# Kernel tuning notes

Hardware: AMD Instinct MI355X
Metric: run time of the kernel (lower is better)

Reference implementation:

```python
import jax, jax.numpy as jnp
import numpy as np

B, S, E = 4, 2048, 1024
H = 4
DH = E // H          # 256 head dim
DQ = E // 4          # 256 quaternion d_model
ALPHA = 1.5
EPS = 1e-10
FOCUS = 0.9
SEL = 2.0


def setup_inputs() -> dict:
    key = jax.random.key(0)
    ks = jax.random.split(key, 6)
    sc = 0.02
    return {
        "x": jax.random.normal(ks[0], (B, S, E), dtype=jnp.float32),
        "in_proj_w": jax.random.normal(ks[1], (3 * E, E), dtype=jnp.float32) * sc,
        "in_proj_b": jnp.zeros((3 * E,), dtype=jnp.float32),
        "out_w": jax.random.normal(ks[2], (E, E), dtype=jnp.float32) * sc,
        "out_b": jnp.zeros((E,), dtype=jnp.float32),
        "m_w1": jax.random.normal(ks[3], (E, E), dtype=jnp.float32) * sc,
        "m_b1": jnp.zeros((E,), dtype=jnp.float32),
        "m_w2": jax.random.normal(ks[4], (E, E), dtype=jnp.float32) * sc,
        "m_b2": jnp.zeros((E,), dtype=jnp.float32),
    }


def quaternion_multiply(q1, q2):
    # Hamilton product over last dim of size 4 (complex-valued components).
    w1, x1, y1, z1 = q1[..., 0], q1[..., 1], q1[..., 2], q1[..., 3]
    w2, x2, y2, z2 = q2[..., 0], q2[..., 1], q2[..., 2], q2[..., 3]
    return jnp.stack([
        w1 * w2 - x1 * x2 - y1 * y2 - z1 * z2,
        w1 * x2 + x1 * w2 + y1 * z2 - z1 * y2,
        w1 * y2 - x1 * z2 + y1 * w2 + z1 * x2,
        w1 * z2 + x1 * y2 - y1 * x2 + z1 * w2,
    ], axis=-1)


def _mha(x, in_proj_w, in_proj_b, out_w, out_b):
    # torch nn.MultiheadAttention self-attention, batch_first
    qkv = x @ in_proj_w.T + in_proj_b              # [B,S,3E]
    q, k, v = jnp.split(qkv, 3, axis=-1)
    q = q.reshape(B, S, H, DH)
    k = k.reshape(B, S, H, DH)
    v = v.reshape(B, S, H, DH)
    scores = jnp.einsum('bqhd,bkhd->bhqk', q, k) / jnp.sqrt(jnp.float32(DH))
    attn = jax.nn.softmax(scores, axis=-1)
    out = jnp.einsum('bhqk,bkhd->bqhd', attn, v).reshape(B, S, E)
    return out @ out_w.T + out_b


def _spectral_attention(signal):
    sq = signal.reshape(B, S, DQ, 4)
    sfft = jnp.fft.fft(sq, axis=-3)                 # complex64, FFT over seq
    kk = jnp.arange(S, dtype=jnp.float32)
    filt = jnp.exp(1j * ALPHA * jnp.arctan(jnp.log(kk + EPS)))  # [S] complex
    sf = sfft * filt[None, :, None, None]
    inter = quaternion_multiply(quaternion_multiply(sf, sf), sf)
    attended = jnp.fft.ifft(inter, axis=-3).real
    return attended.reshape(B, S, E)


def reference(x, in_proj_w, in_proj_b, out_w, out_b, m_w1, m_b1, m_w2, m_b2):
    nicotinic = _mha(x, in_proj_w, in_proj_b, out_w, out_b)
    h = jax.nn.gelu(x @ m_w1.T + m_b1, approximate=False)
    muscarinic = h @ m_w2.T + m_b2
    chol = FOCUS * nicotinic + (1.0 - FOCUS) * muscarinic
    attn_w = _spectral_attention(chol * SEL)
    return x * attn_w
```

## Files before the change

kernel.cpp:

```cpp
#include <hip/hip_runtime.h>
#include <cstdint>

typedef _Float16 f16;
typedef unsigned short u16;
typedef __attribute__((ext_vector_type(8))) _Float16 half8;
typedef __attribute__((ext_vector_type(4))) _Float16 half4;
typedef __attribute__((ext_vector_type(2))) __fp16 fp16x2;
typedef __attribute__((ext_vector_type(4))) float f32x4;

#define MFMA_F16(a, b, c) __builtin_amdgcn_mfma_f32_16x16x32_f16(a, b, c, 0, 0, 0)

#define WAITVM8() asm volatile("s_waitcnt vmcnt(8)" ::: "memory")
#define WAITVM4() asm volatile("s_waitcnt vmcnt(4)" ::: "memory")
#define WAITVM0() asm volatile("s_waitcnt vmcnt(0)" ::: "memory")
#define BARRIER() do { asm volatile("" ::: "memory"); __builtin_amdgcn_s_barrier(); \
                       asm volatile("" ::: "memory"); } while (0)

#define SCQ 0.09016844005555896f

__device__ inline void stage16(const void* g, void* l) {
#if defined(__has_builtin) && __has_builtin(__builtin_amdgcn_global_load_lds)
  __builtin_amdgcn_global_load_lds(
      (const __attribute__((address_space(1))) unsigned*)g,
      (__attribute__((address_space(3))) unsigned*)l, 16, 0, 0);
#else
  *(int4*)l = *(const int4*)g;
#endif
}

__device__ inline int pack_f16(float a, float b) {
#if defined(__has_builtin) && __has_builtin(__builtin_amdgcn_cvt_pkrtz)
  union { fp16x2 h; int i; } u;
  u.h = __builtin_amdgcn_cvt_pkrtz(a, b);
  return u.i;
#else
  union { f16 h[2]; int i; } u;
  u.h[0] = (f16)a; u.h[1] = (f16)b;
  return u.i;
#endif
}

__global__ __launch_bounds__(256)
void conv_all(const float* __restrict__ x, const float* __restrict__ wqkv,
              const float* __restrict__ w1, const float* __restrict__ wout,
              const float* __restrict__ w2, f16* __restrict__ dst,
              float2* __restrict__ tab) {
  if (blockIdx.x >= 7168) {
    int kk = (blockIdx.x - 7168) * 256 + threadIdx.x;
    if (kk < 2048) {
      float s, c;
      sincosf(1.5f * atanf(logf((float)kk + 1e-10f)), &s, &c);
      tab[kk] = make_float2(c, s);
    } else if (kk < 3072) {
      int j = kk - 2048;
      float s, c;
      sincosf(-6.2831853071795864769f * (float)j * (1.0f / 2048.0f), &s, &c);
      tab[kk] = make_float2(c, s);
    }
    return;
  }
  int i = (blockIdx.x * 256 + threadIdx.x) * 8;
  const float* src; size_t dofs; float sc = 1.0f;
  if (i < 8388608)       { src = x + i;               dofs = i; }
  else if (i < 11534336) {
    int t = i - 8388608;
    src = wqkv + t; dofs = i;
    if ((t >> 10) < 1024) sc = SCQ;
  }
  else if (i < 12582912) { src = w1 + (i - 11534336);  dofs = i; }
  else if (i < 13631488) {
    int t = i - 12582912; int j = t >> 10, k = t & 1023;
    src = wout + t; dofs = 12582912 + (size_t)j * 2048 + k; sc = 1.8f;
  } else {
    int t = i - 13631488; int j = t >> 10, k = t & 1023;
    src = w2 + t; dofs = 13631488 - 1048576 + (size_t)j * 2048 + 1024 + k; sc = 0.2f;
  }
  float4 a = *(const float4*)src;
  float4 b = *(const float4*)(src + 4);
  half8 h;
  h[0] = (f16)(a.x * sc); h[1] = (f16)(a.y * sc); h[2] = (f16)(a.z * sc); h[3] = (f16)(a.w * sc);
  h[4] = (f16)(b.x * sc); h[5] = (f16)(b.y * sc); h[6] = (f16)(b.z * sc); h[7] = (f16)(b.w * sc);
  *(half8*)(dst + dofs) = h;
}

template<int EPI>
__global__ __launch_bounds__(256, 2)
void gemm_f16(const f16* __restrict__ A, const f16* __restrict__ W,
              const float* __restrict__ bias0, const float* __restrict__ bias1,
              void* __restrict__ out0, void* __restrict__ out1,
              f16* __restrict__ Vt, int N, int K) {
  __shared__ __align__(16) f16 lds[2][16384];
  const int tid = threadIdx.x;
  const int lane = tid & 63, w = tid >> 6;
  const int g = lane >> 4, lm = lane & 15;
  const int wr = w >> 1, wc = w & 1;
  const int nwg = gridDim.x * gridDim.y;
  const int flat = blockIdx.y * gridDim.x + blockIdx.x;
  const int logical = (flat & 7) * (nwg >> 3) + (flat >> 3);
  const int bx = logical % gridDim.x, by = logical / gridDim.x;
  const int m0 = by * 128, n0 = bx * 128;

  const f16* src[8];
#pragma unroll
  for (int j = 0; j < 8; ++j) {
    int u = j * 256 + tid;
    if (u < 1024) {
      int row = u >> 3, s = u & 7;
      src[j] = A + (size_t)(m0 + row) * K + ((s ^ (row & 7)) << 3);
    } else {
      int v = u - 1024;
      int row = v >> 3, s = v & 7;
      src[j] = W + (size_t)(n0 + row) * K + ((s ^ (row & 7)) << 3);
    }
  }

  f32x4 acc[4][4];
#pragma unroll
  for (int mt = 0; mt < 4; ++mt)
#pragma unroll
    for (int nt = 0; nt < 4; ++nt) acc[mt][nt] = (f32x4){0.f, 0.f, 0.f, 0.f};

#pragma unroll
  for (int j = 0; j < 8; ++j) stage16(src[j], &lds[0][(j * 256 + tid) * 8]);
  __syncthreads();

  const int KT = K >> 6;
#pragma unroll 1
  for (int t = 0; t < KT; ++t) {
    const f16* bufA = lds[t & 1];
    const f16* bufB = bufA + 8192;
    if (t + 1 < KT) {
#pragma unroll
      for (int j = 0; j < 8; ++j) {
        src[j] += 64;
        stage16(src[j], &lds[(t + 1) & 1][(j * 256 + tid) * 8]);
      }
      WAITVM8();
    } else {
      WAITVM0();
    }
    BARRIER();
#pragma unroll
    for (int ks = 0; ks < 2; ++ks) {
      half8 a[4], b[4];
#pragma unroll
      for (int mt = 0; mt < 4; ++mt) {
        int row = wr * 64 + mt * 16 + lm;
        a[mt] = *(const half8*)(bufA + row * 64 + (((ks * 4 + g) ^ (row & 7)) << 3));
      }
#pragma unroll
      for (int nt = 0; nt < 4; ++nt) {
        int row = wc * 64 + nt * 16 + lm;
        b[nt] = *(const half8*)(bufB + row * 64 + (((ks * 4 + g) ^ (row & 7)) << 3));
      }
#pragma unroll
      for (int mt = 0; mt < 4; ++mt)
#pragma unroll
        for (int nt = 0; nt < 4; ++nt)
          acc[mt][nt] = MFMA_F16(a[mt], b[nt], acc[mt][nt]);
    }
    BARRIER();
  }

  const int crow = m0 + wr * 64 + g * 4;
  const int ccol = n0 + wc * 64 + lm;
  if (EPI == 3) {
    if (n0 < 2048) {
      f16* qk = (f16*)out0;
      const float bsc = (n0 < 1024) ? SCQ : 1.0f;
#pragma unroll
      for (int nt = 0; nt < 4; ++nt) {
        float bb = bias0[ccol + nt * 16] * bsc;
#pragma unroll
        for (int mt = 0; mt < 4; ++mt)
#pragma unroll
          for (int r = 0; r < 4; ++r)
            qk[(size_t)(crow + mt * 16 + r) * 3072 + ccol + nt * 16] =
                (f16)(acc[mt][nt][r] + bb);
      }
    } else if (n0 < 3072) {
      f16* ldsT = (f16*)lds;
#pragma unroll
      for (int nt = 0; nt < 4; ++nt) {
        float bb = bias0[ccol + nt * 16];
        int c = wc * 64 + nt * 16 + lm;
#pragma unroll
        for (int mt = 0; mt < 4; ++mt) {
          int r = wr * 64 + mt * 16 + g * 4;
#pragma unroll
          for (int rr = 0; rr < 4; ++rr)
            ldsT[c * 136 + r + rr] = (f16)(acc[mt][nt][rr] + bb);
        }
      }
      BARRIER();
      const int vbase0 = n0 - 2048;
      const int b = m0 >> 11, srow = m0 & 2047;
#pragma unroll
      for (int it = 0; it < 8; ++it) {
        int id = it * 256 + tid;
        int c = id >> 4, rb = id & 15;
        int vcol = vbase0 + c;
        int h = vcol >> 8, d = vcol & 255;
        half8 v = *(half8*)&ldsT[c * 136 + rb * 8];
        *(half8*)&Vt[(((size_t)(b * 4 + h)) * 256 + d) * 2048 + srow + rb * 8] = v;
      }
    } else {
      f16* cat = (f16*)out1;
      const int hc = ccol - 3072;
#pragma unroll
      for (int nt = 0; nt < 4; ++nt) {
        float bb = bias1[hc + nt * 16];
#pragma unroll
        for (int mt = 0; mt < 4; ++mt)
#pragma unroll
          for (int r = 0; r < 4; ++r) {
            float v = acc[mt][nt][r] + bb;
            v = 0.5f * v * (1.0f + erff(v * 0.70710678118654752f));
            cat[(size_t)(crow + mt * 16 + r) * 2048 + 1024 + hc + nt * 16] = (f16)v;
          }
      }
    }
  } else {
    f16* ldsT = (f16*)lds;
#pragma unroll
    for (int nt = 0; nt < 4; ++nt) {
      float bb = 1.8f * bias0[ccol + nt * 16] + 0.2f * bias1[ccol + nt * 16];
      int c = wc * 64 + nt * 16 + lm;
#pragma unroll
      for (int mt = 0; mt < 4; ++mt) {
        int r = wr * 64 + mt * 16 + g * 4;
#pragma unroll
        for (int rr = 0; rr < 4; ++rr)
          ldsT[c * 136 + r + rr] = (f16)(acc[mt][nt][rr] + bb);
      }
    }
    BARRIER();
    f16* ch = (f16*)out0;
#pragma unroll
    for (int it = 0; it < 8; ++it) {
      int id = it * 256 + tid;
      int c = id >> 4, rb = id & 15;
      half8 v = *(half8*)&ldsT[c * 136 + rb * 8];
      *(half8*)&ch[(size_t)(n0 + c) * 8192 + m0 + rb * 8] = v;
    }
  }
}

__global__ __launch_bounds__(512, 1)
void flash_f16(const f16* __restrict__ qkv, const f16* __restrict__ Vt,
               f16* __restrict__ attn) {
  __shared__ __align__(16) f16 lds[65536];
  const int tid = threadIdx.x;
  const int lane = tid & 63, w = tid >> 6;
  const int g = lane >> 4, lm = lane & 15;
  const int raw = blockIdx.x;
  const int bh = (raw & 7) * 2 + (raw >> 7);
  const int qt = (raw >> 3) & 15;
  const int b = bh >> 2, h = bh & 3;
  const int q0 = qt * 128 + w * 16;

  half8 qf[8];
  {
    const f16* qp = qkv + (size_t)(b * 2048 + q0 + lm) * 3072 + h * 256 + g * 8;
#pragma unroll
    for (int c = 0; c < 8; ++c) qf[c] = *(const half8*)(qp + c * 32);
  }

  const f16* kbase = qkv + (size_t)b * 2048 * 3072 + 1024 + h * 256;
  const f16* vbase = Vt + (size_t)bh * 256 * 2048;
  int kofs[4], vofs[4];
#pragma unroll
  for (int j = 0; j < 4; ++j) {
    int u = j * 512 + tid;
    int kv = u >> 5, s = u & 31;
    kofs[j] = kv * 3072 + ((s ^ (kv & 7)) << 3);
    int d = u >> 3, sl = u & 7;
    vofs[j] = d * 2048 + ((sl ^ (d & 7)) << 3);
  }

  f32x4 o[16];
#pragma unroll
  for (int f = 0; f < 16; ++f) o[f] = (f32x4){0.f, 0.f, 0.f, 0.f};
  float m = -3e38f, l = 0.f;
  half8 paP0 = (half8){0, 0, 0, 0, 0, 0, 0, 0};
  half8 paP1 = (half8){0, 0, 0, 0, 0, 0, 0, 0};

#pragma unroll
  for (int j = 0; j < 4; ++j) stage16(kbase + kofs[j], &lds[(j * 512 + tid) * 8]);

#pragma unroll 1
  for (int t = 0; t < 32; ++t) {
    const int cb_ = t & 1;
    if (t < 31) {
      const int kt = (t + 1) * 196608;
#pragma unroll
      for (int j = 0; j < 4; ++j)
        stage16(kbase + kofs[j] + kt, &lds[(cb_ ^ 1) * 16384 + (j * 512 + tid) * 8]);
    }
    {
      const int vt_ = t * 64;
#pragma unroll
      for (int j = 0; j < 4; ++j)
        stage16(vbase + vofs[j] + vt_, &lds[32768 + cb_ * 16384 + (j * 512 + tid) * 8]);
    }
    if (t < 31) { WAITVM8(); } else { WAITVM4(); }
    BARRIER();

    const f16* kb = &lds[cb_ * 16384];

    f32x4 s0 = {0.f, 0.f, 0.f, 0.f}, s1 = {0.f, 0.f, 0.f, 0.f};
    f32x4 s2 = {0.f, 0.f, 0.f, 0.f}, s3 = {0.f, 0.f, 0.f, 0.f};
    __builtin_amdgcn_s_setprio(1);
#pragma unroll
    for (int c = 0; c < 8; ++c) {
      int slot = ((c * 4 + g) ^ (lm & 7)) << 3;
      const f16* kr = kb + lm * 256 + slot;
      half8 b0 = *(const half8*)(kr);
      half8 b1 = *(const half8*)(kr + 16 * 256);
      half8 b2 = *(const half8*)(kr + 32 * 256);
      half8 b3 = *(const half8*)(kr + 48 * 256);
      s0 = MFMA_F16(b0, qf[c], s0);
      s1 = MFMA_F16(b1, qf[c], s1);
      s2 = MFMA_F16(b2, qf[c], s2);
      s3 = MFMA_F16(b3, qf[c], s3);
    }
    __builtin_amdgcn_s_setprio(0);

    if (t > 0) {
      const f16* vbp = &lds[32768 + (cb_ ^ 1) * 16384];
      __builtin_amdgcn_s_setprio(1);
#pragma unroll
      for (int f = 0; f < 16; ++f) {
        int d = f * 16 + lm;
        const f16* vr = vbp + d * 64;
        half8 bv0 = *(const half8*)(vr + ((g ^ (d & 7)) << 3));
        half8 bv1 = *(const half8*)(vr + (((4 + g) ^ (d & 7)) << 3));
        o[f] = MFMA_F16(paP0, bv0, o[f]);
        o[f] = MFMA_F16(paP1, bv1, o[f]);
      }
      __builtin_amdgcn_s_setprio(0);
    }

    float mx = fmaxf(fmaxf(fmaxf(s0[0], s0[1]), fmaxf(s0[2], s0[3])),
                     fmaxf(fmaxf(s1[0], s1[1]), fmaxf(s1[2], s1[3])));
    mx = fmaxf(mx, fmaxf(fmaxf(fmaxf(s2[0], s2[1]), fmaxf(s2[2], s2[3])),
                         fmaxf(fmaxf(s3[0], s3[1]), fmaxf(s3[2], s3[3]))));
    mx = fmaxf(mx, __shfl_xor(mx, 16));
    mx = fmaxf(mx, __shfl_xor(mx, 32));

    if (!__all(mx <= m + 8.0f)) {
      float mn = fmaxf(m, mx);
      float corr = exp2f(m - mn);
      m = mn; l *= corr;
#pragma unroll
      for (int r = 0; r < 4; ++r) {
        float cr = __shfl(corr, ((lane >> 2) & 12) + r);
#pragma unroll
        for (int f = 0; f < 16; ++f) o[f][r] *= cr;
      }
    }

    float e0[4], e1[4], e2[4], e3[4];
#pragma unroll
    for (int r = 0; r < 4; ++r) {
      e0[r] = exp2f(s0[r] - m);
      e1[r] = exp2f(s1[r] - m);
      e2[r] = exp2f(s2[r] - m);
      e3[r] = exp2f(s3[r] - m);
    }
    float rs = ((e0[0] + e0[1]) + (e0[2] + e0[3])) + ((e1[0] + e1[1]) + (e1[2] + e1[3]))
             + ((e2[0] + e2[1]) + (e2[2] + e2[3])) + ((e3[0] + e3[1]) + (e3[2] + e3[3]));
    rs += __shfl_xor(rs, 16);
    rs += __shfl_xor(rs, 32);
    l += rs;

    const int s1l = ((lane & 16) << 1) + lm;
    const int s2l = s1l + 16;
    const bool hi = lane >= 32;
    {
      int A01 = pack_f16(e0[0], e0[1]);
      int A23 = pack_f16(e0[2], e0[3]);
      int B01 = pack_f16(e1[0], e1[1]);
      int B23 = pack_f16(e1[2], e1[3]);
      int t0a = __shfl(A01, s1l), t0b = __shfl(B01, s1l);
      int t1a = __shfl(A23, s1l), t1b = __shfl(B23, s1l);
      int t2a = __shfl(A01, s2l), t2b = __shfl(B01, s2l);
      int t3a = __shfl(A23, s2l), t3b = __shfl(B23, s2l);
      union { int i[4]; half8 h; } pau;
      pau.i[0] = hi ? t0b : t0a;
      pau.i[1] = hi ? t1b : t1a;
      pau.i[2] = hi ? t2b : t2a;
      pau.i[3] = hi ? t3b : t3a;
      paP0 = pau.h;
    }
    {
      int A01 = pack_f16(e2[0], e2[1]);
      int A23 = pack_f16(e2[2], e2[3]);
      int B01 = pack_f16(e3[0], e3[1]);
      int B23 = pack_f16(e3[2], e3[3]);
      int t0a = __shfl(A01, s1l), t0b = __shfl(B01, s1l);
      int t1a = __shfl(A23, s1l), t1b = __shfl(B23, s1l);
      int t2a = __shfl(A01, s2l), t2b = __shfl(B01, s2l);
      int t3a = __shfl(A23, s2l), t3b = __shfl(B23, s2l);
      union { int i[4]; half8 h; } pau;
      pau.i[0] = hi ? t0b : t0a;
      pau.i[1] = hi ? t1b : t1a;
      pau.i[2] = hi ? t2b : t2a;
      pau.i[3] = hi ? t3b : t3a;
      paP1 = pau.h;
    }

    BARRIER();
  }

  WAITVM0();
  BARRIER();
  {
    const f16* vbp = &lds[32768 + 16384];
#pragma unroll
    for (int f = 0; f < 16; ++f) {
      int d = f * 16 + lm;
      const f16* vr = vbp + d * 64;
      half8 bv0 = *(const half8*)(vr + ((g ^ (d & 7)) << 3));
      half8 bv1 = *(const half8*)(vr + (((4 + g) ^ (d & 7)) << 3));
      o[f] = MFMA_F16(paP0, bv0, o[f]);
      o[f] = MFMA_F16(paP1, bv1, o[f]);
    }
  }

  float inv[4];
#pragma unroll
  for (int r = 0; r < 4; ++r) inv[r] = 1.0f / __shfl(l, ((lane >> 2) & 12) + r);
#pragma unroll
  for (int f = 0; f < 16; ++f)
#pragma unroll
    for (int r = 0; r < 4; ++r)
      attn[(size_t)(b * 2048 + q0 + g * 4 + r) * 2048 + h * 256 + f * 16 + lm] =
          (f16)(o[f][r] * inv[r]);
}

__device__ inline float2 cmul(float2 a, float2 b) {
  return make_float2(a.x * b.x - a.y * b.y, a.x * b.y + a.y * b.x);
}
__device__ inline float2 cmulc(float2 a, float2 b) {
  return make_float2(a.x * b.x + a.y * b.y, a.y * b.x - a.x * b.y);
}
__device__ inline void qcube(float2& w, float2& x, float2& y, float2& z, float2 f) {
  w = cmul(w, f); x = cmul(x, f); y = cmul(y, f); z = cmul(z, f);
  float2 a2 = cmul(w, w);
  float2 sx = cmul(x, x), sy = cmul(y, y), sz = cmul(z, z);
  float2 s = make_float2(sx.x + sy.x + sz.x, sx.y + sy.y + sz.y);
  float2 t3 = make_float2(a2.x - 3.f * s.x, a2.y - 3.f * s.y);
  float2 cf = make_float2(3.f * a2.x - s.x, 3.f * a2.y - s.y);
  w = cmul(w, t3); x = cmul(cf, x); y = cmul(cf, y); z = cmul(cf, z);
}

__device__ inline int fftpos(int k) {
  int kp = k >> 1;
  return ((k & 1) << 10) | ((kp & 3) << 8) | ((kp & 12) << 4) | (kp & 48)
       | ((kp >> 4) & 12) | ((kp >> 8) & 3);
}

__global__ __launch_bounds__(256)
void spectral7(const f16* __restrict__ cholT, const float* __restrict__ xin,
               const float2* __restrict__ tab, float* __restrict__ outp) {
  __shared__ __align__(16) float2 Z[2][2048];
  __shared__ float2 tw[1024];
  const int tid = threadIdx.x;
  const int b = blockIdx.x >> 8;
  const int qd = blockIdx.x & 255;
  const size_t c0 = (size_t)qd * 4;
  const f16* t0 = cholT + (c0 + 0) * 8192 + b * 2048;
  const f16* t1 = cholT + (c0 + 1) * 8192 + b * 2048;
  const f16* t2 = cholT + (c0 + 2) * 8192 + b * 2048;
  const f16* t3 = cholT + (c0 + 3) * 8192 + b * 2048;
  const float2* ftab = tab;
  const float2* twt = tab + 2048;

  for (int j = tid; j < 1024; j += 256) tw[j] = twt[j];
  for (int s = tid; s < 1024; s += 256) {
    float2 z0a = make_float2((float)t0[s], (float)t1[s]);
    float2 z1a = make_float2((float)t2[s], (float)t3[s]);
    float2 z0b = make_float2((float)t0[s + 1024], (float)t1[s + 1024]);
    float2 z1b = make_float2((float)t2[s + 1024], (float)t3[s + 1024]);
    float2 w = twt[s];
    Z[0][s] = make_float2(z0a.x + z0b.x, z0a.y + z0b.y);
    Z[0][s + 1024] = cmul(make_float2(z0a.x - z0b.x, z0a.y - z0b.y), w);
    Z[1][s] = make_float2(z1a.x + z1b.x, z1a.y + z1b.y);
    Z[1][s + 1024] = cmul(make_float2(z1a.x - z1b.x, z1a.y - z1b.y), w);
  }
  __syncthreads();

#pragma unroll 1
  for (int lq = 8; lq >= 0; lq -= 2) {
    const int Q = 1 << lq, st = 512 >> lq;
#pragma unroll 1
    for (int it = 0; it < 4; ++it) {
      int gg = it * 256 + tid;
      int c = gg >> 9, bf = gg & 511;
      int j = bf & (Q - 1);
      int base = ((bf >> lq) << (lq + 2)) | j;
      float2 a = Z[c][base], bq = Z[c][base + Q];
      float2 cc = Z[c][base + 2 * Q], d = Z[c][base + 3 * Q];
      float2 t0_ = make_float2(a.x + cc.x, a.y + cc.y);
      float2 t1_ = make_float2(a.x - cc.x, a.y - cc.y);
      float2 t2_ = make_float2(bq.x + d.x, bq.y + d.y);
      float2 bd = make_float2(bq.x - d.x, bq.y - d.y);
      float2 t3_ = make_float2(bd.y, -bd.x);
      float2 y0 = make_float2(t0_.x + t2_.x, t0_.y + t2_.y);
      float2 y1 = make_float2(t1_.x + t3_.x, t1_.y + t3_.y);
      float2 y2 = make_float2(t0_.x - t2_.x, t0_.y - t2_.y);
      float2 y3 = make_float2(t1_.x - t3_.x, t1_.y - t3_.y);
      int i3 = 3 * j * st;
      float sg = (i3 & 1024) ? -1.f : 1.f;
      i3 &= 1023;
      Z[c][base] = y0;
      Z[c][base + Q] = cmul(y1, tw[j * st]);
      Z[c][base + 2 * Q] = cmul(y2, tw[2 * j * st]);
      float2 r3 = cmul(y3, tw[i3]);
      Z[c][base + 3 * Q] = make_float2(r3.x * sg, r3.y * sg);
    }
    __syncthreads();
  }

#pragma unroll 1
  for (int it = 0; it < 4; ++it) {
    int jj = it * 256 + tid;
    int nrep = (jj == 0) ? 2 : 1;
#pragma unroll 1
    for (int rep = 0; rep < nrep; ++rep) {
      int k  = (jj == 0) ? (rep ? 1024 : 0) : jj;
      int kn = (jj == 0) ? k : 2048 - jj;
      int p  = fftpos(k);
      int pp = fftpos(kn);
      float2 z0p = Z[0][p], z0q = Z[0][pp];
      float2 z1p = Z[1][p], z1q = Z[1][pp];
      float2 wk = make_float2(0.5f * (z0p.x + z0q.x), 0.5f * (z0p.y - z0q.y));
      float2 xk = make_float2(0.5f * (z0p.y + z0q.y), 0.5f * (z0q.x - z0p.x));
      float2 yk = make_float2(0.5f * (z1p.x + z1q.x), 0.5f * (z1p.y - z1q.y));
      float2 zk = make_float2(0.5f * (z1p.y + z1q.y), 0.5f * (z1q.x - z1p.x));
      float2 wn = make_float2(0.5f * (z0q.x + z0p.x), 0.5f * (z0q.y - z0p.y));
      float2 xn = make_float2(0.5f * (z0q.y + z0p.y), 0.5f * (z0p.x - z0q.x));
      float2 yn = make_float2(0.5f * (z1q.x + z1p.x), 0.5f * (z1q.y - z1p.y));
      float2 zn = make_float2(0.5f * (z1q.y + z1p.y), 0.5f * (z1p.x - z1q.x));
      float2 fk = ftab[k], fn = ftab[kn];
      qcube(wk, xk, yk, zk, fk);
      qcube(wn, xn, yn, zn, fn);
      Z[0][p]  = make_float2(0.5f * (wk.x + wn.x) - 0.5f * (xk.y - xn.y),
                             0.5f * (wk.y - wn.y) + 0.5f * (xk.x + xn.x));
      Z[0][pp] = make_float2(0.5f * (wn.x + wk.x) - 0.5f * (xn.y - xk.y),
                             0.5f * (wn.y - wk.y) + 0.5f * (xn.x + xk.x));
      Z[1][p]  = make_float2(0.5f * (yk.x + yn.x) - 0.5f * (zk.y - zn.y),
                             0.5f * (yk.y - yn.y) + 0.5f * (zk.x + zn.x));
      Z[1][pp] = make_float2(0.5f * (yn.x + yk.x) - 0.5f * (zn.y - zk.y),
                             0.5f * (yn.y - yk.y) + 0.5f * (zn.x + zk.x));
    }
  }
  __syncthreads();

#pragma unroll 1
  for (int lq = 0; lq <= 8; lq += 2) {
    const int Q = 1 << lq, st = 512 >> lq;
#pragma unroll 1
    for (int it = 0; it < 4; ++it) {
      int gg = it * 256 + tid;
      int c = gg >> 9, bf = gg & 511;
      int j = bf & (Q - 1);
      int base = ((bf >> lq) << (lq + 2)) | j;
      float2 a = Z[c][base];
      float2 bq = cmulc(Z[c][base + Q], tw[j * st]);
      float2 cc = cmulc(Z[c][base + 2 * Q], tw[2 * j * st]);
      int i3 = 3 * j * st;
      float sg = (i3 & 1024) ? -1.f : 1.f;
      i3 &= 1023;
      float2 d = cmulc(Z[c][base + 3 * Q], tw[i3]);
      d = make_float2(d.x * sg, d.y * sg);
      float2 t0_ = make_float2(a.x + cc.x, a.y + cc.y);
      float2 t1_ = make_float2(a.x - cc.x, a.y - cc.y);
      float2 t2_ = make_float2(bq.x + d.x, bq.y + d.y);
      float2 bd = make_float2(bq.x - d.x, bq.y - d.y);
      float2 t3_ = make_float2(-bd.y, bd.x);
      Z[c][base]         = make_float2(t0_.x + t2_.x, t0_.y + t2_.y);
      Z[c][base + Q]     = make_float2(t1_.x + t3_.x, t1_.y + t3_.y);
      Z[c][base + 2 * Q] = make_float2(t0_.x - t2_.x, t0_.y - t2_.y);
      Z[c][base + 3 * Q] = make_float2(t1_.x - t3_.x, t1_.y - t3_.y);
    }
    __syncthreads();
  }

  const float* xb = xin + (size_t)b * 2048 * 1024;
  float* ob = outp + (size_t)b * 2048 * 1024;
  const float inv = 1.0f / 2048.0f;
  for (int j = tid; j < 1024; j += 256) {
    float2 wj = tw[j];
    float2 a0 = Z[0][j], bw0 = cmulc(Z[0][j + 1024], wj);
    float2 a1 = Z[1][j], bw1 = cmulc(Z[1][j + 1024], wj);
    float2 r0lo = make_float2(a0.x + bw0.x, a0.y + bw0.y);
    float2 r0hi = make_float2(a0.x - bw0.x, a0.y - bw0.y);
    float2 r1lo = make_float2(a1.x + bw1.x, a1.y + bw1.y);
    float2 r1hi = make_float2(a1.x - bw1.x, a1.y - bw1.y);
    float4 xlo = *(const float4*)(xb + (size_t)j * 1024 + c0);
    float4 xhi = *(const float4*)(xb + (size_t)(j + 1024) * 1024 + c0);
    float4 olo, ohi;
    olo.x = xlo.x * r0lo.x * inv;
    olo.y = xlo.y * r0lo.y * inv;
    olo.z = xlo.z * r1lo.x * inv;
    olo.w = xlo.w * r1lo.y * inv;
    ohi.x = xhi.x * r0hi.x * inv;
    ohi.y = xhi.y * r0hi.y * inv;
    ohi.z = xhi.z * r1hi.x * inv;
    ohi.w = xhi.w * r1hi.y * inv;
    *(float4*)(ob + (size_t)j * 1024 + c0) = olo;
    *(float4*)(ob + (size_t)(j + 1024) * 1024 + c0) = ohi;
  }
}

extern "C" void kernel_launch(void* const* d_in, const int* in_sizes, int n_in,
                              void* d_out, int out_size, void* d_ws, size_t ws_size,
                              hipStream_t stream) {
  const float* x    = (const float*)d_in[0];
  const float* wqkv = (const float*)d_in[1];
  const float* bqkv = (const float*)d_in[2];
  const float* wout = (const float*)d_in[3];
  const float* bout = (const float*)d_in[4];
  const float* w1   = (const float*)d_in[5];
  const float* b1   = (const float*)d_in[6];
  const float* w2   = (const float*)d_in[7];
  const float* b2   = (const float*)d_in[8];
  float* out = (float*)d_out;
  char* wsb = (char*)d_ws;
  const size_t MB = 1048576;

  f16*   xf    = (f16*)(wsb);
  f16*   wqf   = (f16*)(wsb + 16 * MB);
  f16*   wcat  = (f16*)(wsb + 24 * MB);
  f16*   qkvF  = (f16*)(wsb + 32 * MB);
  f16*   VtF   = (f16*)(wsb + 80 * MB);
  f16*   cat   = (f16*)(wsb + 96 * MB);
  f16*   cholT = (f16*)(wsb + 128 * MB);
  float2* tab  = (float2*)(wsb + 145 * MB);

  conv_all<<<7184, 256, 0, stream>>>(x, wqkv, w1, wout, w2, xf, tab);

  gemm_f16<3><<<dim3(32, 64), 256, 0, stream>>>(xf, wqf, bqkv, b1, qkvF, cat, VtF, 4096, 1024);
  flash_f16<<<256, 512, 0, stream>>>(qkvF, VtF, cat);
  gemm_f16<4><<<dim3(8, 64), 256, 0, stream>>>(cat, wcat, bout, b2, cholT, nullptr, nullptr, 1024, 2048);
  spectral7<<<1024, 256, 0, stream>>>(cholT, x, tab, out);
}
```

Before: 342.0 us.

## Process two 16-row query tiles per wave in flash attention with 256 threads

Each wave in the flash attention kernel now handles 32 query rows as two 16-row sub-tiles. Every K and V fragment read from LDS is reused across two MFMAs, and the block shrinks from 512 to 256 threads with twice the staging loads per thread. This halves LDS read traffic per FLOP, but doubles accumulator and Q-fragment registers per wave (about 128 fp32 accumulators plus 16 half8 Q) and leaves fewer waves per CU to hide latency. The grid keeps 256 blocks, so each block still covers 128 queries.

```diff
diff --git a/kernel.cpp b/kernel.cpp
--- a/kernel.cpp
+++ b/kernel.cpp
@@ -10,9 +10,9 @@
 
 #define MFMA_F16(a, b, c) __builtin_amdgcn_mfma_f32_16x16x32_f16(a, b, c, 0, 0, 0)
 
-#define WAITVM8() asm volatile("s_waitcnt vmcnt(8)" ::: "memory")
-#define WAITVM4() asm volatile("s_waitcnt vmcnt(4)" ::: "memory")
-#define WAITVM0() asm volatile("s_waitcnt vmcnt(0)" ::: "memory")
+#define WAITVM16() asm volatile("s_waitcnt vmcnt(16)" ::: "memory")
+#define WAITVM8()  asm volatile("s_waitcnt vmcnt(8)" ::: "memory")
+#define WAITVM0()  asm volatile("s_waitcnt vmcnt(0)" ::: "memory")
 #define BARRIER() do { asm volatile("" ::: "memory"); __builtin_amdgcn_s_barrier(); \
                        asm volatile("" ::: "memory"); } while (0)
 
@@ -246,7 +246,7 @@
   }
 }
 
-__global__ __launch_bounds__(512, 1)
+__global__ __launch_bounds__(256)
 void flash_f16(const f16* __restrict__ qkv, const f16* __restrict__ Vt,
                f16* __restrict__ attn) {
   __shared__ __align__(16) f16 lds[65536];
@@ -257,36 +257,43 @@
   const int bh = (raw & 7) * 2 + (raw >> 7);
   const int qt = (raw >> 3) & 15;
   const int b = bh >> 2, h = bh & 3;
-  const int q0 = qt * 128 + w * 16;
-
-  half8 qf[8];
+  const int q0 = qt * 128 + w * 32;
+
+  half8 qfA[8], qfB[8];
   {
-    const f16* qp = qkv + (size_t)(b * 2048 + q0 + lm) * 3072 + h * 256 + g * 8;
-#pragma unroll
-    for (int c = 0; c < 8; ++c) qf[c] = *(const half8*)(qp + c * 32);
+    const f16* qpA = qkv + (size_t)(b * 2048 + q0 + lm) * 3072 + h * 256 + g * 8;
+    const f16* qpB = qpA + (size_t)16 * 3072;
+#pragma unroll
+    for (int c = 0; c < 8; ++c) {
+      qfA[c] = *(const half8*)(qpA + c * 32);
+      qfB[c] = *(const half8*)(qpB + c * 32);
+    }
   }
 
   const f16* kbase = qkv + (size_t)b * 2048 * 3072 + 1024 + h * 256;
   const f16* vbase = Vt + (size_t)bh * 256 * 2048;
-  int kofs[4], vofs[4];
-#pragma unroll
-  for (int j = 0; j < 4; ++j) {
-    int u = j * 512 + tid;
+  int kofs[8], vofs[8];
+#pragma unroll
+  for (int j = 0; j < 8; ++j) {
+    int u = j * 256 + tid;
     int kv = u >> 5, s = u & 31;
     kofs[j] = kv * 3072 + ((s ^ (kv & 7)) << 3);
     int d = u >> 3, sl = u & 7;
     vofs[j] = d * 2048 + ((sl ^ (d & 7)) << 3);
   }
 
-  f32x4 o[16];
-#pragma unroll
-  for (int f = 0; f < 16; ++f) o[f] = (f32x4){0.f, 0.f, 0.f, 0.f};
-  float m = -3e38f, l = 0.f;
-  half8 paP0 = (half8){0, 0, 0, 0, 0, 0, 0, 0};
-  half8 paP1 = (half8){0, 0, 0, 0, 0, 0, 0, 0};
-
-#pragma unroll
-  for (int j = 0; j < 4; ++j) stage16(kbase + kofs[j], &lds[(j * 512 + tid) * 8]);
+  f32x4 oA[16], oB[16];
+#pragma unroll
+  for (int f = 0; f < 16; ++f) {
+    oA[f] = (f32x4){0.f, 0.f, 0.f, 0.f};
+    oB[f] = (f32x4){0.f, 0.f, 0.f, 0.f};
+  }
+  float mA = -3e38f, lA = 0.f, mB = -3e38f, lB = 0.f;
+  half8 paA0 = (half8){0,0,0,0,0,0,0,0}, paA1 = (half8){0,0,0,0,0,0,0,0};
+  half8 paB0 = (half8){0,0,0,0,0,0,0,0}, paB1 = (half8){0,0,0,0,0,0,0,0};
+
+#pragma unroll
+  for (int j = 0; j < 8; ++j) stage16(kbase + kofs[j], &lds[(j * 256 + tid) * 8]);
 
 #pragma unroll 1
   for (int t = 0; t < 32; ++t) {
@@ -294,22 +301,22 @@
     if (t < 31) {
       const int kt = (t + 1) * 196608;
 #pragma unroll
-      for (int j = 0; j < 4; ++j)
-        stage16(kbase + kofs[j] + kt, &lds[(cb_ ^ 1) * 16384 + (j * 512 + tid) * 8]);
+      for (int j = 0; j < 8; ++j)
+        stage16(kbase + kofs[j] + kt, &lds[(cb_ ^ 1) * 16384 + (j * 256 + tid) * 8]);
     }
     {
       const int vt_ = t * 64;
 #pragma unroll
-      for (int j = 0; j < 4; ++j)
-        stage16(vbase + vofs[j] + vt_, &lds[32768 + cb_ * 16384 + (j * 512 + tid) * 8]);
-    }
-    if (t < 31) { WAITVM8(); } else { WAITVM4(); }
+      for (int j = 0; j < 8; ++j)
+        stage16(vbase + vofs[j] + vt_, &lds[32768 + cb_ * 16384 + (j * 256 + tid) * 8]);
+    }
+    if (t < 31) { WAITVM16(); } else { WAITVM8(); }
     BARRIER();
 
     const f16* kb = &lds[cb_ * 16384];
 
-    f32x4 s0 = {0.f, 0.f, 0.f, 0.f}, s1 = {0.f, 0.f, 0.f, 0.f};
-    f32x4 s2 = {0.f, 0.f, 0.f, 0.f}, s3 = {0.f, 0.f, 0.f, 0.f};
+    f32x4 sA0 = {0,0,0,0}, sA1 = {0,0,0,0}, sA2 = {0,0,0,0}, sA3 = {0,0,0,0};
+    f32x4 sB0 = {0,0,0,0}, sB1 = {0,0,0,0}, sB2 = {0,0,0,0}, sB3 = {0,0,0,0};
     __builtin_amdgcn_s_setprio(1);
 #pragma unroll
     for (int c = 0; c < 8; ++c) {
@@ -319,10 +326,14 @@
       half8 b1 = *(const half8*)(kr + 16 * 256);
       half8 b2 = *(const half8*)(kr + 32 * 256);
       half8 b3 = *(const half8*)(kr + 48 * 256);
-      s0 = MFMA_F16(b0, qf[c], s0);
-      s1 = MFMA_F16(b1, qf[c], s1);
-      s2 = MFMA_F16(b2, qf[c], s2);
-      s3 = MFMA_F16(b3, qf[c], s3);
+      sA0 = MFMA_F16(b0, qfA[c], sA0);
+      sB0 = MFMA_F16(b0, qfB[c], sB0);
+      sA1 = MFMA_F16(b1, qfA[c], sA1);
+      sB1 = MFMA_F16(b1, qfB[c], sB1);
+      sA2 = MFMA_F16(b2, qfA[c], sA2);
+      sB2 = MFMA_F16(b2, qfB[c], sB2);
+      sA3 = MFMA_F16(b3, qfA[c], sA3);
+      sB3 = MFMA_F16(b3, qfB[c], sB3);
     }
     __builtin_amdgcn_s_setprio(0);
 
@@ -335,79 +346,150 @@
         const f16* vr = vbp + d * 64;
         half8 bv0 = *(const half8*)(vr + ((g ^ (d & 7)) << 3));
         half8 bv1 = *(const half8*)(vr + (((4 + g) ^ (d & 7)) << 3));
-        o[f] = MFMA_F16(paP0, bv0, o[f]);
-        o[f] = MFMA_F16(paP1, bv1, o[f]);
+        oA[f] = MFMA_F16(paA0, bv0, oA[f]);
+        oB[f] = MFMA_F16(paB0, bv0, oB[f]);
+        oA[f] = MFMA_F16(paA1, bv1, oA[f]);
+        oB[f] = MFMA_F16(paB1, bv1, oB[f]);
       }
       __builtin_amdgcn_s_setprio(0);
     }
 
-    float mx = fmaxf(fmaxf(fmaxf(s0[0], s0[1]), fmaxf(s0[2], s0[3])),
-                     fmaxf(fmaxf(s1[0], s1[1]), fmaxf(s1[2], s1[3])));
-    mx = fmaxf(mx, fmaxf(fmaxf(fmaxf(s2[0], s2[1]), fmaxf(s2[2], s2[3])),
-                         fmaxf(fmaxf(s3[0], s3[1]), fmaxf(s3[2], s3[3]))));
-    mx = fmaxf(mx, __shfl_xor(mx, 16));
-    mx = fmaxf(mx, __shfl_xor(mx, 32));
-
-    if (!__all(mx <= m + 8.0f)) {
-      float mn = fmaxf(m, mx);
-      float corr = exp2f(m - mn);
-      m = mn; l *= corr;
+    {
+      float mx = fmaxf(fmaxf(fmaxf(sA0[0], sA0[1]), fmaxf(sA0[2], sA0[3])),
+                       fmaxf(fmaxf(sA1[0], sA1[1]), fmaxf(sA1[2], sA1[3])));
+      mx = fmaxf(mx, fmaxf(fmaxf(fmaxf(sA2[0], sA2[1]), fmaxf(sA2[2], sA2[3])),
+                           fmaxf(fmaxf(sA3[0], sA3[1]), fmaxf(sA3[2], sA3[3]))));
+      mx = fmaxf(mx, __shfl_xor(mx, 16));
+      mx = fmaxf(mx, __shfl_xor(mx, 32));
+      if (!__all(mx <= mA + 8.0f)) {
+        float mn = fmaxf(mA, mx);
+        float corr = exp2f(mA - mn);
+        mA = mn; lA *= corr;
+#pragma unroll
+        for (int r = 0; r < 4; ++r) {
+          float cr = __shfl(corr, ((lane >> 2) & 12) + r);
+#pragma unroll
+          for (int f = 0; f < 16; ++f) oA[f][r] *= cr;
+        }
+      }
+      float e0[4], e1[4], e2[4], e3[4];
 #pragma unroll
       for (int r = 0; r < 4; ++r) {
-        float cr = __shfl(corr, ((lane >> 2) & 12) + r);
-#pragma unroll
-        for (int f = 0; f < 16; ++f) o[f][r] *= cr;
-      }
-    }
-
-    float e0[4], e1[4], e2[4], e3[4];
-#pragma unroll
-    for (int r = 0; r < 4; ++r) {
-      e0[r] = exp2f(s0[r] - m);
-      e1[r] = exp2f(s1[r] - m);
-      e2[r] = exp2f(s2[r] - m);
-      e3[r] = exp2f(s3[r] - m);
-    }
-    float rs = ((e0[0] + e0[1]) + (e0[2] + e0[3])) + ((e1[0] + e1[1]) + (e1[2] + e1[3]))
-             + ((e2[0] + e2[1]) + (e2[2] + e2[3])) + ((e3[0] + e3[1]) + (e3[2] + e3[3]));
-    rs += __shfl_xor(rs, 16);
-    rs += __shfl_xor(rs, 32);
-    l += rs;
-
-    const int s1l = ((lane & 16) << 1) + lm;
-    const int s2l = s1l + 16;
-    const bool hi = lane >= 32;
+        e0[r] = exp2f(sA0[r] - mA);
+        e1[r] = exp2f(sA1[r] - mA);
+        e2[r] = exp2f(sA2[r] - mA);
+        e3[r] = exp2f(sA3[r] - mA);
+      }
+      float rs = ((e0[0]+e0[1])+(e0[2]+e0[3])) + ((e1[0]+e1[1])+(e1[2]+e1[3]))
+               + ((e2[0]+e2[1])+(e2[2]+e2[3])) + ((e3[0]+e3[1])+(e3[2]+e3[3]));
+      rs += __shfl_xor(rs, 16);
+      rs += __shfl_xor(rs, 32);
+      lA += rs;
+
+      const int s1l = ((lane & 16) << 1) + lm;
+      const int s2l = s1l + 16;
+      const bool hi = lane >= 32;
+      {
+        int A01 = pack_f16(e0[0], e0[1]);
+        int A23 = pack_f16(e0[2], e0[3]);
+        int B01 = pack_f16(e1[0], e1[1]);
+        int B23 = pack_f16(e1[2], e1[3]);
+        int t0a = __shfl(A01, s1l), t0b = __shfl(B01, s1l);
+        int t1a = __shfl(A23, s1l), t1b = __shfl(B23, s1l);
+        int t2a = __shfl(A01, s2l), t2b = __shfl(B01, s2l);
+        int t3a = __shfl(A23, s2l), t3b = __shfl(B23, s2l);
+        union { int i[4]; half8 h; } pau;
+        pau.i[0] = hi ? t0b : t0a;
+        pau.i[1] = hi ? t1b : t1a;
+        pau.i[2] = hi ? t2b : t2a;
+        pau.i[3] = hi ? t3b : t3a;
+        paA0 = pau.h;
+      }
+      {
+        int A01 = pack_f16(e2[0], e2[1]);
+        int A23 = pack_f16(e2[2], e2[3]);
+        int B01 = pack_f16(e3[0], e3[1]);
+        int B23 = pack_f16(e3[2], e3[3]);
+        int t0a = __shfl(A01, s1l), t0b = __shfl(B01, s1l);
+        int t1a = __shfl(A23, s1l), t1b = __shfl(B23, s1l);
+        int t2a = __shfl(A01, s2l), t2b = __shfl(B01, s2l);
+        int t3a = __shfl(A23, s2l), t3b = __shfl(B23, s2l);
+        union { int i[4]; half8 h; } pau;
+        pau.i[0] = hi ? t0b : t0a;
+        pau.i[1] = hi ? t1b : t1a;
+        pau.i[2] = hi ? t2b : t2a;
+        pau.i[3] = hi ? t3b : t3a;
+        paA1 = pau.h;
+      }
+    }
+
     {
-      int A01 = pack_f16(e0[0], e0[1]);
-      int A23 = pack_f16(e0[2], e0[3]);
-      int B01 = pack_f16(e1[0], e1[1]);
-      int B23 = pack_f16(e1[2], e1[3]);
-      int t0a = __shfl(A01, s1l), t0b = __shfl(B01, s1l);
-      int t1a = __shfl(A23, s1l), t1b = __shfl(B23, s1l);
-      int t2a = __shfl(A01, s2l), t2b = __shfl(B01, s2l);
-      int t3a = __shfl(A23, s2l), t3b = __shfl(B23, s2l);
-      union { int i[4]; half8 h; } pau;
-      pau.i[0] = hi ? t0b : t0a;
-      pau.i[1] = hi ? t1b : t1a;
-      pau.i[2] = hi ? t2b : t2a;
-      pau.i[3] = hi ? t3b : t3a;
-      paP0 = pau.h;
-    }
-    {
-      int A01 = pack_f16(e2[0], e2[1]);
-      int A23 = pack_f16(e2[2], e2[3]);
-      int B01 = pack_f16(e3[0], e3[1]);
-      int B23 = pack_f16(e3[2], e3[3]);
-      int t0a = __shfl(A01, s1l), t0b = __shfl(B01, s1l);
-      int t1a = __shfl(A23, s1l), t1b = __shfl(B23, s1l);
-      int t2a = __shfl(A01, s2l), t2b = __shfl(B01, s2l);
-      int t3a = __shfl(A23, s2l), t3b = __shfl(B23, s2l);
-      union { int i[4]; half8 h; } pau;
-      pau.i[0] = hi ? t0b : t0a;
-      pau.i[1] = hi ? t1b : t1a;
-      pau.i[2] = hi ? t2b : t2a;
-      pau.i[3] = hi ? t3b : t3a;
-      paP1 = pau.h;
+      float mx = fmaxf(fmaxf(fmaxf(sB0[0], sB0[1]), fmaxf(sB0[2], sB0[3])),
+                       fmaxf(fmaxf(sB1[0], sB1[1]), fmaxf(sB1[2], sB1[3])));
+      mx = fmaxf(mx, fmaxf(fmaxf(fmaxf(sB2[0], sB2[1]), fmaxf(sB2[2], sB2[3])),
+                           fmaxf(fmaxf(sB3[0], sB3[1]), fmaxf(sB3[2], sB3[3]))));
+      mx = fmaxf(mx, __shfl_xor(mx, 16));
+      mx = fmaxf(mx, __shfl_xor(mx, 32));
+      if (!__all(mx <= mB + 8.0f)) {
+        float mn = fmaxf(mB, mx);
+        float corr = exp2f(mB - mn);
+        mB = mn; lB *= corr;
+#pragma unroll
+        for (int r = 0; r < 4; ++r) {
+          float cr = __shfl(corr, ((lane >> 2) & 12) + r);
+#pragma unroll
+          for (int f = 0; f < 16; ++f) oB[f][r] *= cr;
+        }
+      }
+      float e0[4], e1[4], e2[4], e3[4];
+#pragma unroll
+      for (int r = 0; r < 4; ++r) {
+        e0[r] = exp2f(sB0[r] - mB);
+        e1[r] = exp2f(sB1[r] - mB);
+        e2[r] = exp2f(sB2[r] - mB);
+        e3[r] = exp2f(sB3[r] - mB);
+      }
+      float rs = ((e0[0]+e0[1])+(e0[2]+e0[3])) + ((e1[0]+e1[1])+(e1[2]+e1[3]))
+               + ((e2[0]+e2[1])+(e2[2]+e2[3])) + ((e3[0]+e3[1])+(e3[2]+e3[3]));
+      rs += __shfl_xor(rs, 16);
+      rs += __shfl_xor(rs, 32);
+      lB += rs;
+
+      const int s1l = ((lane & 16) << 1) + lm;
+      const int s2l = s1l + 16;
+      const bool hi = lane >= 32;
+      {
+        int A01 = pack_f16(e0[0], e0[1]);
+        int A23 = pack_f16(e0[2], e0[3]);
+        int B01 = pack_f16(e1[0], e1[1]);
+        int B23 = pack_f16(e1[2], e1[3]);
+        int t0a = __shfl(A01, s1l), t0b = __shfl(B01, s1l);
+        int t1a = __shfl(A23, s1l), t1b = __shfl(B23, s1l);
+        int t2a = __shfl(A01, s2l), t2b = __shfl(B01, s2l);
+        int t3a = __shfl(A23, s2l), t3b = __shfl(B23, s2l);
+        union { int i[4]; half8 h; } pau;
+        pau.i[0] = hi ? t0b : t0a;
+        pau.i[1] = hi ? t1b : t1a;
+        pau.i[2] = hi ? t2b : t2a;
+        pau.i[3] = hi ? t3b : t3a;
+        paB0 = pau.h;
+      }
+      {
+        int A01 = pack_f16(e2[0], e2[1]);
+        int A23 = pack_f16(e2[2], e2[3]);
+        int B01 = pack_f16(e3[0], e3[1]);
+        int B23 = pack_f16(e3[2], e3[3]);
+        int t0a = __shfl(A01, s1l), t0b = __shfl(B01, s1l);
+        int t1a = __shfl(A23, s1l), t1b = __shfl(B23, s1l);
+        int t2a = __shfl(A01, s2l), t2b = __shfl(B01, s2l);
+        int t3a = __shfl(A23, s2l), t3b = __shfl(B23, s2l);
+        union { int i[4]; half8 h; } pau;
+        pau.i[0] = hi ? t0b : t0a;
+        pau.i[1] = hi ? t1b : t1a;
+        pau.i[2] = hi ? t2b : t2a;
+        pau.i[3] = hi ? t3b : t3a;
+        paB1 = pau.h;
+      }
     }
 
     BARRIER();
@@ -423,20 +505,27 @@
       const f16* vr = vbp + d * 64;
       half8 bv0 = *(const half8*)(vr + ((g ^ (d & 7)) << 3));
       half8 bv1 = *(const half8*)(vr + (((4 + g) ^ (d & 7)) << 3));
-      o[f] = MFMA_F16(paP0, bv0, o[f]);
-      o[f] = MFMA_F16(paP1, bv1, o[f]);
-    }
-  }
-
-  float inv[4];
-#pragma unroll
-  for (int r = 0; r < 4; ++r) inv[r] = 1.0f / __shfl(l, ((lane >> 2) & 12) + r);
+      oA[f] = MFMA_F16(paA0, bv0, oA[f]);
+      oB[f] = MFMA_F16(paB0, bv0, oB[f]);
+      oA[f] = MFMA_F16(paA1, bv1, oA[f]);
+      oB[f] = MFMA_F16(paB1, bv1, oB[f]);
+    }
+  }
+
+  float invA[4], invB[4];
+#pragma unroll
+  for (int r = 0; r < 4; ++r) {
+    invA[r] = 1.0f / __shfl(lA, ((lane >> 2) & 12) + r);
+    invB[r] = 1.0f / __shfl(lB, ((lane >> 2) & 12) + r);
+  }
 #pragma unroll
   for (int f = 0; f < 16; ++f)
 #pragma unroll
-    for (int r = 0; r < 4; ++r)
-      attn[(size_t)(b * 2048 + q0 + g * 4 + r) * 2048 + h * 256 + f * 16 + lm] =
-          (f16)(o[f][r] * inv[r]);
+    for (int r = 0; r < 4; ++r) {
+      size_t rowA = (size_t)(b * 2048 + q0 + g * 4 + r) * 2048 + h * 256 + f * 16 + lm;
+      attn[rowA] = (f16)(oA[f][r] * invA[r]);
+      attn[rowA + (size_t)16 * 2048] = (f16)(oB[f][r] * invB[r]);
+    }
 }
 
 __device__ inline float2 cmul(float2 a, float2 b) {
@@ -643,7 +732,7 @@
   conv_all<<<7184, 256, 0, stream>>>(x, wqkv, w1, wout, w2, xf, tab);
 
   gemm_f16<3><<<dim3(32, 64), 256, 0, stream>>>(xf, wqf, bqkv, b1, qkvF, cat, VtF, 4096, 1024);
-  flash_f16<<<256, 512, 0, stream>>>(qkvF, VtF, cat);
+  flash_f16<<<256, 256, 0, stream>>>(qkvF, VtF, cat);
   gemm_f16<4><<<dim3(8, 64), 256, 0, stream>>>(cat, wcat, bout, b2, cholT, nullptr, nullptr, 1024, 2048);
   spectral7<<<1024, 256, 0, stream>>>(cholT, x, tab, out);
 }
```

New measurement: 358.0 us. +4.7%, slower.
